# Optimization experiments

Hardware: AMD Instinct MI355X
Metric: run time of the kernel (lower is better)

Reference implementation:

```python
import jax, jax.numpy as jnp
import numpy as np

N_NODES = 100000


def _sage_conv(x, src, dst, W_l, b_l, W_r, n_nodes):
    # mean-aggregate neighbor features: messages flow src -> dst
    msg = x[src]                                              # [E, d]
    agg_sum = jax.ops.segment_sum(msg, dst, num_segments=n_nodes)   # [N, d]
    cnt = jax.ops.segment_sum(jnp.ones((src.shape[0],), x.dtype), dst,
                              num_segments=n_nodes)           # [N]
    agg = agg_sum / jnp.maximum(cnt, 1.0)[:, None]            # mean, 0 for isolated nodes
    return agg @ W_l + b_l + x @ W_r                          # lin_l(agg) + lin_r(x)


def setup_inputs() -> dict:
    key = jax.random.key(0)
    ks = jax.random.split(key, 8)
    in_c, hid_c, out_c = 64, 128, 64
    n_edges = 1000000
    x = jax.random.normal(ks[0], (N_NODES, in_c), dtype=jnp.float32)
    edge_index = jax.random.randint(ks[1], (2, n_edges), 0, N_NODES, dtype=jnp.int32)
    def glorot(k, shape):
        lim = float(np.sqrt(6.0 / (shape[0] + shape[1])))
        return jax.random.uniform(k, shape, jnp.float32, -lim, lim)
    return {
        "x": x,
        "edge_index": edge_index,
        "W_l1": glorot(ks[2], (in_c, hid_c)),
        "b_l1": jnp.zeros((hid_c,), jnp.float32),
        "W_r1": glorot(ks[3], (in_c, hid_c)),
        "W_l2": glorot(ks[4], (hid_c, out_c)),
        "b_l2": jnp.zeros((out_c,), jnp.float32),
        "W_r2": glorot(ks[5], (hid_c, out_c)),
    }


def reference(x, edge_index, W_l1, b_l1, W_r1, W_l2, b_l2, W_r2):
    src, dst = edge_index[0], edge_index[1]
    # eval mode: dropout(p=0.5) is identity
    h = _sage_conv(x, src, dst, W_l1, b_l1, W_r1, N_NODES)
    h = jax.nn.relu(h)
    out = _sage_conv(h, src, dst, W_l2, b_l2, W_r2, N_NODES)
    return out
```

## Files before the change

kernel.cpp:

```cpp
#include <hip/hip_runtime.h>


#define NPB 128
#define NBK 782
#define BCAP_E 1600
#define BCAP_S 2048

typedef __attribute__((ext_vector_type(8))) short bf16x8;
typedef __attribute__((ext_vector_type(4))) float f32x4;
typedef __attribute__((ext_vector_type(4))) int int4v;

__device__ __forceinline__ float bf2f(unsigned short u) {
  return __uint_as_float(((unsigned)u) << 16);
}
__device__ __forceinline__ unsigned short f2bf(float f) {
  unsigned x = __float_as_uint(f);
  x += 0x7fffu + ((x >> 16) & 1u);
  return (unsigned short)(x >> 16);
}

__global__ __launch_bounds__(256) void prep_all(
    const float* __restrict__ x, unsigned short* __restrict__ xb, int total4,
    const float* __restrict__ Wl1, const float* __restrict__ Wr1,
    const float* __restrict__ Wl2, const float* __restrict__ Wr2,
    unsigned short* __restrict__ Wt1, unsigned short* __restrict__ Wcat,
    unsigned short* __restrict__ tzero,
    const int* __restrict__ src, const int* __restrict__ dst,
    int* __restrict__ gcnt, int* __restrict__ ebuf, int e,
    int n, int CB) {
  __shared__ int lcnt[NBK], lbase[NBK];
  int b = blockIdx.x;
  if (b < CB) {
    int i = b * 256 + threadIdx.x;
    if (i < total4) {
      float4 v = ((const float4*)x)[i];
      ushort4 o;
      o.x = f2bf(v.x); o.y = f2bf(v.y); o.z = f2bf(v.z); o.w = f2bf(v.w);
      ((ushort4*)xb)[i] = o;
    }
    return;
  }
  if (b < CB + 128) {
    int o = (b - CB) * 256 + threadIdx.x;
    if (o < 16384) {
      int m = o >> 13, rem = o & 8191;
      int col = rem >> 6, k = rem & 63;
      const float* W = m ? Wr1 : Wl1;
      Wt1[o] = f2bf(W[k * 128 + col]);
    } else {
      int o2 = o - 16384;
      int col = o2 >> 7, k = o2 & 127;
      float v = (col < 64) ? Wl2[k * 64 + col] : Wr2[k * 64 + col - 64];
      Wcat[o2] = f2bf(v);
    }
    return;
  }
  if (b < CB + 129) {
    if (threadIdx.x < 32) {
      ((unsigned*)(xb + (size_t)n * 64))[threadIdx.x] = 0;
      ((unsigned*)(tzero + (size_t)n * 64))[threadIdx.x] = 0;
    }
    return;
  }
  int bb = b - (CB + 129);
  for (int i = threadIdx.x; i < NBK; i += 256) lcnt[i] = 0;
  __syncthreads();
  int pk[16], bk[16];
  int nv = 0;
  int base = bb * 4096 + threadIdx.x * 4;
#pragma unroll
  for (int c = 0; c < 4; ++c) {
    int i = base + c * 1024;
    if (i + 4 <= e) {
      int4v sv = *(const int4v*)(src + i);
      int4v dv = *(const int4v*)(dst + i);
#pragma unroll
      for (int j = 0; j < 4; ++j) {
        bk[nv] = dv[j] >> 7;
        pk[nv] = ((dv[j] & 127) << 17) | sv[j];
        ++nv;
      }
    } else if (i < e) {
      for (int i2 = i; i2 < e; ++i2) {
        int dj = dst[i2], sj = src[i2];
        bk[nv] = dj >> 7;
        pk[nv] = ((dj & 127) << 17) | sj;
        ++nv;
      }
    }
  }
  for (int k = 0; k < nv; ++k) atomicAdd(&lcnt[bk[k]], 1);
  __syncthreads();
  for (int i = threadIdx.x; i < NBK; i += 256) {
    lbase[i] = atomicAdd(&gcnt[i], lcnt[i]);
    lcnt[i] = 0;
  }
  __syncthreads();
  for (int k = 0; k < nv; ++k) {
    int off = lbase[bk[k]] + atomicAdd(&lcnt[bk[k]], 1);
    if (off < BCAP_E) ebuf[bk[k] * BCAP_E + off] = pk[k];
  }
}

__global__ __launch_bounds__(512) void sort_gather_gemm1(
    const unsigned short* __restrict__ xb, const int* __restrict__ gcnt,
    const int* __restrict__ ebuf, const unsigned short* __restrict__ Wt1,
    const float* __restrict__ b1,
    int* __restrict__ srcS, int* __restrict__ nstart, int* __restrict__ ncnt,
    unsigned short* __restrict__ h, int n) {
  __shared__ unsigned short sW[16384];
  __shared__ unsigned short sA[8192];
  __shared__ int sorted[BCAP_S];
  __shared__ int cnt[NPB], cur[NPB], st[NPB + 1];
  int tid = threadIdx.x, lane = tid & 63, wid = tid >> 6;
  int l15 = lane & 15, g = lane >> 4;
  int b = blockIdx.x;

#pragma unroll
  for (int it = 0; it < 4; ++it) {
    int i = it * 512 + tid;
    int byte = i << 4;
    int col = (byte >> 7) & 127;
    int koff = (byte & 127) ^ ((col & 7) << 4);
    int dstb = (byte & ~127) | koff;
    bf16x8 v = *(const bf16x8*)(Wt1 + i * 8);
    *(bf16x8*)((char*)sW + dstb) = v;
  }
  float bj[8];
#pragma unroll
  for (int cb = 0; cb < 8; ++cb) bj[cb] = b1[cb * 16 + l15];

  if (tid < NPB) { cnt[tid] = 0; cur[tid] = 0; }
  __syncthreads();
  int ecnt = min(gcnt[b], BCAP_E);
  const int* eb = ebuf + b * BCAP_E;
  for (int i = tid; i < ecnt; i += 512) atomicAdd(&cnt[eb[i] >> 17], 1);
  __syncthreads();
  if (wid == 0) {
    int i0 = (cnt[lane] + 3) & ~3, i1 = (cnt[64 + lane] + 3) & ~3;
#pragma unroll
    for (int off = 1; off < 64; off <<= 1) {
      int u = __shfl_up(i0, off);
      if (lane >= off) i0 += u;
    }
    int t0 = __shfl(i0, 63);
#pragma unroll
    for (int off = 1; off < 64; off <<= 1) {
      int u = __shfl_up(i1, off);
      if (lane >= off) i1 += u;
    }
    st[lane + 1] = i0;
    st[64 + lane + 1] = t0 + i1;
    if (lane == 0) st[0] = 0;
  }
  __syncthreads();
  for (int i = tid; i < ecnt; i += 512) {
    int pk = eb[i];
    int dl = pk >> 17;
    int pos = st[dl] + atomicAdd(&cur[dl], 1);
    if (pos < BCAP_S) sorted[pos] = pk & 0x1FFFF;
  }
  __syncthreads();
  if (tid < NPB) {
    int c = cnt[tid], p = (c + 3) & ~3;
    int base = st[tid];
    for (int k = c; k < p; ++k)
      if (base + k < BCAP_S) sorted[base + k] = n;
    int node = b * NPB + tid;
    if (node < n) {
      nstart[node] = b * BCAP_S + base;
      ncnt[node] = c;
    }
  }
  __syncthreads();
  int total = min(st[NPB], BCAP_S);
  for (int i = tid; i < total; i += 512) srcS[b * BCAP_S + i] = sorted[i];

  {
    int half32 = lane & 32;
    int hlane = lane & 31;
    int gg = hlane >> 3;
    int ch8 = lane & 7;
#pragma unroll 1
    for (int pass = 0; pass < 8; ++pass) {
      int dl = pass * 16 + wid * 2 + (lane >> 5);
      int s = st[dl], c = cnt[dl];
      int dpad = (c + 3) & ~3;
      float acc[8];
#pragma unroll
      for (int j = 0; j < 8; ++j) acc[j] = 0.f;
      int nit = dpad >> 2;
      int nitw = max(nit, __shfl_xor(nit, 32));
      int idx = (s + hlane < BCAP_S) ? sorted[s + hlane] : n;
      bf16x8 cch[8];
#pragma unroll
      for (int u = 0; u < 8; ++u) {
        if (u < nitw) {
          int r = u * 4 + gg;
          int sidx = __shfl(idx, half32 + r);
          if (u < nit) cch[u] = *(const bf16x8*)(xb + (size_t)sidx * 64 + ch8 * 8);
        }
      }
#pragma unroll
      for (int u = 0; u < 8; ++u) {
        if (u < nitw && u < nit) {
#pragma unroll
          for (int j = 0; j < 8; ++j) acc[j] += bf2f((unsigned short)cch[u][j]);
        }
      }
      for (int b0 = 32; b0 < dpad; b0 += 32) {
        int idx2 = (s + b0 + hlane < BCAP_S) ? sorted[s + b0 + hlane] : n;
#pragma unroll
        for (int u = 0; u < 8; ++u) {
          int r = u * 4 + gg;
          if (b0 + r < dpad) {
            int sidx = __shfl(idx2, half32 + r);
            bf16x8 v = *(const bf16x8*)(xb + (size_t)sidx * 64 + ch8 * 8);
#pragma unroll
            for (int j = 0; j < 8; ++j) acc[j] += bf2f((unsigned short)v[j]);
          }
        }
      }
#pragma unroll
      for (int m = 8; m < 32; m <<= 1) {
#pragma unroll
        for (int j = 0; j < 8; ++j) acc[j] += __shfl_xor(acc[j], m);
      }
      if (hlane < 8) {
        float inv = 1.f / (float)max(c, 1);
        bf16x8 o;
#pragma unroll
        for (int j = 0; j < 8; ++j) o[j] = (short)f2bf(acc[j] * inv);
        int byte = dl * 128 + ((ch8 * 16) ^ ((dl & 7) << 4));
        *(bf16x8*)((char*)sA + byte) = o;
      }
    }
  }
  __syncthreads();

  int rowl = wid * 16 + l15;
  int growbase = b * 128 + wid * 16;
  size_t cr = (size_t)min(growbase + l15, n - 1);

  f32x4 acc[8];
#pragma unroll
  for (int cb = 0; cb < 8; ++cb) acc[cb] = (f32x4){0.f, 0.f, 0.f, 0.f};

#pragma unroll
  for (int m = 0; m < 2; ++m) {
#pragma unroll
    for (int s = 0; s < 2; ++s) {
      int ko = s * 64 + g * 16;
      bf16x8 a;
      if (m == 0) {
        int koff = ko ^ ((rowl & 7) << 4);
        a = *(const bf16x8*)((const char*)sA + rowl * 128 + koff);
      } else {
        a = *(const bf16x8*)((const char*)xb + cr * 128 + ko);
      }
#pragma unroll
      for (int cb = 0; cb < 8; ++cb) {
        int col = cb * 16 + l15;
        int koff = ko ^ ((col & 7) << 4);
        bf16x8 bb = *(const bf16x8*)((const char*)sW + m * 16384 + col * 128 + koff);
        acc[cb] = __builtin_amdgcn_mfma_f32_16x16x32_bf16(a, bb, acc[cb], 0, 0, 0);
      }
    }
  }
  int rb = growbase + g * 4;
#pragma unroll
  for (int r = 0; r < 4; ++r) {
    int row = rb + r;
    if (row < n) {
      unsigned short* hp = h + (size_t)row * 128 + l15;
#pragma unroll
      for (int cb = 0; cb < 8; ++cb) {
        float v = fmaxf(acc[cb][r] + bj[cb], 0.f);
        hp[cb * 16] = f2bf(v);
      }
    }
  }
}

__global__ __launch_bounds__(256) void gemm2_mfma(
    const unsigned short* __restrict__ h, const unsigned short* __restrict__ Wcat,
    const float* __restrict__ b2, unsigned short* __restrict__ t,
    float* __restrict__ outp, int n) {
  __shared__ unsigned short sW[16384];
  int tid = threadIdx.x;
  int lane = tid & 63, wid = tid >> 6;
  int l15 = lane & 15, g = lane >> 4;
#pragma unroll
  for (int it = 0; it < 8; ++it) {
    int i = it * 256 + tid;
    int byte = i << 4;
    int col = byte >> 8;
    int koff = (byte & 255) ^ ((col & 15) << 4);
    int dstb = (byte & ~255) | koff;
    bf16x8 v = *(const bf16x8*)(Wcat + i * 8);
    *(bf16x8*)((char*)sW + dstb) = v;
  }
  float bj[4];
#pragma unroll
  for (int cb = 0; cb < 4; ++cb) bj[cb] = b2[cb * 16 + l15];
  __syncthreads();

  int rowbase = blockIdx.x * 128 + wid * 32;
  int r0 = rowbase + l15, r1 = r0 + 16;
  size_t cr0 = (size_t)min(r0, n - 1), cr1 = (size_t)min(r1, n - 1);

  f32x4 acc[2][8];
#pragma unroll
  for (int fr = 0; fr < 2; ++fr)
#pragma unroll
    for (int cb = 0; cb < 8; ++cb) acc[fr][cb] = (f32x4){0.f, 0.f, 0.f, 0.f};

  const char* hb = (const char*)h;
#pragma unroll
  for (int s = 0; s < 4; ++s) {
    int ko = s * 64 + g * 16;
    bf16x8 a0 = *(const bf16x8*)(hb + cr0 * 256 + ko);
    bf16x8 a1 = *(const bf16x8*)(hb + cr1 * 256 + ko);
#pragma unroll
    for (int cb = 0; cb < 8; ++cb) {
      int col = cb * 16 + l15;
      int koff = ko ^ ((col & 15) << 4);
      bf16x8 b = *(const bf16x8*)((const char*)sW + col * 256 + koff);
      acc[0][cb] = __builtin_amdgcn_mfma_f32_16x16x32_bf16(a0, b, acc[0][cb], 0, 0, 0);
      acc[1][cb] = __builtin_amdgcn_mfma_f32_16x16x32_bf16(a1, b, acc[1][cb], 0, 0, 0);
    }
  }
#pragma unroll
  for (int fr = 0; fr < 2; ++fr) {
    int rb = rowbase + fr * 16 + g * 4;
#pragma unroll
    for (int r = 0; r < 4; ++r) {
      int row = rb + r;
      if (row < n) {
#pragma unroll
        for (int cb = 0; cb < 4; ++cb)
          t[(size_t)row * 64 + cb * 16 + l15] = f2bf(acc[fr][cb][r]);
#pragma unroll
        for (int cb = 0; cb < 4; ++cb)
          outp[(size_t)row * 64 + cb * 16 + l15] = acc[fr][cb + 4][r] + bj[cb];
      }
    }
  }
}

__device__ __forceinline__ void gather2(
    const unsigned short* __restrict__ feat, const int* __restrict__ srcS,
    int s, int dpad, int lane, float* acc) {
  int half32 = lane & 32;
  int hlane = lane & 31;
  int g = hlane >> 3;
  int ch8 = lane & 7;
#pragma unroll
  for (int j = 0; j < 8; ++j) acc[j] = 0.f;
  int nit = dpad >> 2;
  int nitw = max(nit, __shfl_xor(nit, 32));
  int idx = srcS[s + hlane];
  bf16x8 c[8];
#pragma unroll
  for (int u = 0; u < 8; ++u) {
    if (u < nitw) {
      int r = u * 4 + g;
      int sidx = __shfl(idx, half32 + r);
      if (u < nit) c[u] = *(const bf16x8*)(feat + (size_t)sidx * 64 + ch8 * 8);
    }
  }
#pragma unroll
  for (int u = 0; u < 8; ++u) {
    if (u < nitw && u < nit) {
#pragma unroll
      for (int j = 0; j < 8; ++j) acc[j] += bf2f((unsigned short)c[u][j]);
    }
  }
  for (int b0 = 32; b0 < dpad; b0 += 32) {
    int idx2 = srcS[s + b0 + hlane];
#pragma unroll
    for (int u = 0; u < 8; ++u) {
      int r = u * 4 + g;
      if (b0 + r < dpad) {
        int sidx = __shfl(idx2, half32 + r);
        bf16x8 v = *(const bf16x8*)(feat + (size_t)sidx * 64 + ch8 * 8);
#pragma unroll
        for (int j = 0; j < 8; ++j) acc[j] += bf2f((unsigned short)v[j]);
      }
    }
  }
#pragma unroll
  for (int m = 8; m < 32; m <<= 1) {
#pragma unroll
    for (int j = 0; j < 8; ++j) acc[j] += __shfl_xor(acc[j], m);
  }
}

__global__ __launch_bounds__(256) void agg_add_fast(
    const unsigned short* __restrict__ feat, const int* __restrict__ nstart,
    const int* __restrict__ ncnt, const int* __restrict__ srcS,
    float* __restrict__ outp, int n) {
  int lane = threadIdx.x & 63, wid = threadIdx.x >> 6;
  int half = lane >> 5;
  int node = (blockIdx.x * 4 + wid) * 2 + half;
  bool live = node < n;
  int cn = live ? node : n - 1;
  int s = nstart[cn];
  int c = ncnt[cn];
  int dpad = (c + 3) & ~3;
  float acc[8];
  gather2(feat, srcS, s, dpad, lane, acc);
  float inv = 1.f / (float)max(c, 1);
  if ((lane & 31) < 8 && live) {
    float4* op = (float4*)(outp + (size_t)node * 64 + (lane & 7) * 8);
    float4 o0 = op[0], o1 = op[1];
    o0.x += acc[0] * inv; o0.y += acc[1] * inv;
    o0.z += acc[2] * inv; o0.w += acc[3] * inv;
    o1.x += acc[4] * inv; o1.y += acc[5] * inv;
    o1.z += acc[6] * inv; o1.w += acc[7] * inv;
    op[0] = o0; op[1] = o1;
  }
}

extern "C" void kernel_launch(void* const* d_in, const int* in_sizes, int n_in,
                              void* d_out, int out_size, void* d_ws, size_t ws_size,
                              hipStream_t stream) {
  const float* x   = (const float*)d_in[0];
  const int*   ei  = (const int*)d_in[1];
  const float* Wl1 = (const float*)d_in[2];
  const float* b1  = (const float*)d_in[3];
  const float* Wr1 = (const float*)d_in[4];
  const float* Wl2 = (const float*)d_in[5];
  const float* b2  = (const float*)d_in[6];
  const float* Wr2 = (const float*)d_in[7];
  float* out = (float*)d_out;

  const int n = in_sizes[0] / 64;
  const int e = in_sizes[1] / 2;
  const int* src = ei;
  const int* dst = ei + e;

  char* ws = (char*)d_ws;
  size_t off = 0;
  auto take = [&](size_t bytes) { void* p = ws + off; off = (off + bytes + 255) & ~(size_t)255; return p; };
  int*            gcnt   = (int*)take((size_t)NBK * 4);
  int*            ebuf   = (int*)take((size_t)NBK * BCAP_E * 4);
  int*            srcS   = (int*)take((size_t)NBK * BCAP_S * 4 + 256);
  int*            nstart = (int*)take((size_t)n * 4);
  int*            ncnt   = (int*)take((size_t)n * 4);
  unsigned short* xb     = (unsigned short*)take(((size_t)n + 1) * 64 * 2);
  unsigned short* t      = (unsigned short*)take(((size_t)n + 1) * 64 * 2);
  unsigned short* h      = (unsigned short*)take((size_t)n * 128 * 2);
  unsigned short* Wt1    = (unsigned short*)take(16384 * 2);
  unsigned short* Wcat   = (unsigned short*)take(16384 * 2);

  const int total4 = n * 64 / 4;
  const int CB = (total4 + 255) / 256;
  const int EB2 = (e + 4095) / 4096;

  (void)hipMemsetAsync(gcnt, 0, (size_t)NBK * 4, stream);
  prep_all<<<CB + 129 + EB2, 256, 0, stream>>>(x, xb, total4,
                                               Wl1, Wr1, Wl2, Wr2, Wt1, Wcat,
                                               t, src, dst, gcnt, ebuf, e, n, CB);
  sort_gather_gemm1<<<NBK, 512, 0, stream>>>(xb, gcnt, ebuf, Wt1, b1,
                                             srcS, nstart, ncnt, h, n);
  gemm2_mfma<<<NBK, 256, 0, stream>>>(h, Wcat, b2, t, out, n);
  agg_add_fast<<<(n + 7) / 8, 256, 0, stream>>>(t, nstart, ncnt, srcS, out, n);
}
```

Measured before the change: 124.0 us.

## Split bucketize and per-bucket sort into separate kernels, fold memset into prep

```diff
diff --git a/kernel.cpp b/kernel.cpp
--- a/kernel.cpp
+++ b/kernel.cpp
@@ -19,16 +19,13 @@
   return (unsigned short)(x >> 16);
 }
 
-__global__ __launch_bounds__(256) void prep_all(
+__global__ __launch_bounds__(256) void fused_misc(
     const float* __restrict__ x, unsigned short* __restrict__ xb, int total4,
     const float* __restrict__ Wl1, const float* __restrict__ Wr1,
     const float* __restrict__ Wl2, const float* __restrict__ Wr2,
     unsigned short* __restrict__ Wt1, unsigned short* __restrict__ Wcat,
-    unsigned short* __restrict__ tzero,
-    const int* __restrict__ src, const int* __restrict__ dst,
-    int* __restrict__ gcnt, int* __restrict__ ebuf, int e,
+    int* __restrict__ gcnt, unsigned short* __restrict__ tzero,
     int n, int CB) {
-  __shared__ int lcnt[NBK], lbase[NBK];
   int b = blockIdx.x;
   if (b < CB) {
     int i = b * 256 + threadIdx.x;
@@ -38,9 +35,7 @@
       o.x = f2bf(v.x); o.y = f2bf(v.y); o.z = f2bf(v.z); o.w = f2bf(v.w);
       ((ushort4*)xb)[i] = o;
     }
-    return;
-  }
-  if (b < CB + 128) {
+  } else if (b < CB + 128) {
     int o = (b - CB) * 256 + threadIdx.x;
     if (o < 16384) {
       int m = o >> 13, rem = o & 8191;
@@ -53,21 +48,24 @@
       float v = (col < 64) ? Wl2[k * 64 + col] : Wr2[k * 64 + col - 64];
       Wcat[o2] = f2bf(v);
     }
-    return;
-  }
-  if (b < CB + 129) {
+  } else {
+    for (int i = threadIdx.x; i < NBK; i += 256) gcnt[i] = 0;
     if (threadIdx.x < 32) {
       ((unsigned*)(xb + (size_t)n * 64))[threadIdx.x] = 0;
       ((unsigned*)(tzero + (size_t)n * 64))[threadIdx.x] = 0;
     }
-    return;
-  }
-  int bb = b - (CB + 129);
+  }
+}
+
+__global__ __launch_bounds__(256) void bucketize(
+    const int* __restrict__ src, const int* __restrict__ dst,
+    int* __restrict__ gcnt, int* __restrict__ ebuf, int e) {
+  __shared__ int lcnt[NBK], lbase[NBK];
   for (int i = threadIdx.x; i < NBK; i += 256) lcnt[i] = 0;
   __syncthreads();
   int pk[16], bk[16];
   int nv = 0;
-  int base = bb * 4096 + threadIdx.x * 4;
+  int base = blockIdx.x * 4096 + threadIdx.x * 4;
 #pragma unroll
   for (int c = 0; c < 4; ++c) {
     int i = base + c * 1024;
@@ -102,16 +100,69 @@
   }
 }
 
-__global__ __launch_bounds__(512) void sort_gather_gemm1(
-    const unsigned short* __restrict__ xb, const int* __restrict__ gcnt,
-    const int* __restrict__ ebuf, const unsigned short* __restrict__ Wt1,
-    const float* __restrict__ b1,
+__global__ __launch_bounds__(256) void sort_write(
+    const int* __restrict__ gcnt, const int* __restrict__ ebuf,
     int* __restrict__ srcS, int* __restrict__ nstart, int* __restrict__ ncnt,
+    int n) {
+  __shared__ int cnt[NPB], cur[NPB], st[NPB + 1], sorted[BCAP_S];
+  int tid = threadIdx.x, lane = tid & 63, wid = tid >> 6;
+  int b = blockIdx.x;
+  if (tid < NPB) { cnt[tid] = 0; cur[tid] = 0; }
+  __syncthreads();
+  int ecnt = min(gcnt[b], BCAP_E);
+  const int* eb = ebuf + b * BCAP_E;
+  for (int i = tid; i < ecnt; i += 256) atomicAdd(&cnt[eb[i] >> 17], 1);
+  __syncthreads();
+  if (wid == 0) {
+    int i0 = (cnt[lane] + 3) & ~3, i1 = (cnt[64 + lane] + 3) & ~3;
+#pragma unroll
+    for (int off = 1; off < 64; off <<= 1) {
+      int u = __shfl_up(i0, off);
+      if (lane >= off) i0 += u;
+    }
+    int t0 = __shfl(i0, 63);
+#pragma unroll
+    for (int off = 1; off < 64; off <<= 1) {
+      int u = __shfl_up(i1, off);
+      if (lane >= off) i1 += u;
+    }
+    st[lane + 1] = i0;
+    st[64 + lane + 1] = t0 + i1;
+    if (lane == 0) st[0] = 0;
+  }
+  __syncthreads();
+  for (int i = tid; i < ecnt; i += 256) {
+    int pk = eb[i];
+    int dl = pk >> 17;
+    int pos = st[dl] + atomicAdd(&cur[dl], 1);
+    if (pos < BCAP_S) sorted[pos] = pk & 0x1FFFF;
+  }
+  __syncthreads();
+  if (tid < NPB) {
+    int c = cnt[tid], p = (c + 3) & ~3;
+    int base = st[tid];
+    for (int k = c; k < p; ++k)
+      if (base + k < BCAP_S) sorted[base + k] = n;
+  }
+  __syncthreads();
+  int total = min(st[NPB], BCAP_S);
+  for (int i = tid; i < total; i += 256) srcS[b * BCAP_S + i] = sorted[i];
+  if (tid < NPB) {
+    int node = b * NPB + tid;
+    if (node < n) {
+      nstart[node] = b * BCAP_S + st[tid];
+      ncnt[node] = cnt[tid];
+    }
+  }
+}
+
+__global__ __launch_bounds__(512) void gather_gemm1(
+    const unsigned short* __restrict__ xb, const int* __restrict__ nstart,
+    const int* __restrict__ ncnt, const int* __restrict__ srcS,
+    const unsigned short* __restrict__ Wt1, const float* __restrict__ b1,
     unsigned short* __restrict__ h, int n) {
   __shared__ unsigned short sW[16384];
   __shared__ unsigned short sA[8192];
-  __shared__ int sorted[BCAP_S];
-  __shared__ int cnt[NPB], cur[NPB], st[NPB + 1];
   int tid = threadIdx.x, lane = tid & 63, wid = tid >> 6;
   int l15 = lane & 15, g = lane >> 4;
   int b = blockIdx.x;
@@ -130,52 +181,6 @@
 #pragma unroll
   for (int cb = 0; cb < 8; ++cb) bj[cb] = b1[cb * 16 + l15];
 
-  if (tid < NPB) { cnt[tid] = 0; cur[tid] = 0; }
-  __syncthreads();
-  int ecnt = min(gcnt[b], BCAP_E);
-  const int* eb = ebuf + b * BCAP_E;
-  for (int i = tid; i < ecnt; i += 512) atomicAdd(&cnt[eb[i] >> 17], 1);
-  __syncthreads();
-  if (wid == 0) {
-    int i0 = (cnt[lane] + 3) & ~3, i1 = (cnt[64 + lane] + 3) & ~3;
-#pragma unroll
-    for (int off = 1; off < 64; off <<= 1) {
-      int u = __shfl_up(i0, off);
-      if (lane >= off) i0 += u;
-    }
-    int t0 = __shfl(i0, 63);
-#pragma unroll
-    for (int off = 1; off < 64; off <<= 1) {
-      int u = __shfl_up(i1, off);
-      if (lane >= off) i1 += u;
-    }
-    st[lane + 1] = i0;
-    st[64 + lane + 1] = t0 + i1;
-    if (lane == 0) st[0] = 0;
-  }
-  __syncthreads();
-  for (int i = tid; i < ecnt; i += 512) {
-    int pk = eb[i];
-    int dl = pk >> 17;
-    int pos = st[dl] + atomicAdd(&cur[dl], 1);
-    if (pos < BCAP_S) sorted[pos] = pk & 0x1FFFF;
-  }
-  __syncthreads();
-  if (tid < NPB) {
-    int c = cnt[tid], p = (c + 3) & ~3;
-    int base = st[tid];
-    for (int k = c; k < p; ++k)
-      if (base + k < BCAP_S) sorted[base + k] = n;
-    int node = b * NPB + tid;
-    if (node < n) {
-      nstart[node] = b * BCAP_S + base;
-      ncnt[node] = c;
-    }
-  }
-  __syncthreads();
-  int total = min(st[NPB], BCAP_S);
-  for (int i = tid; i < total; i += 512) srcS[b * BCAP_S + i] = sorted[i];
-
   {
     int half32 = lane & 32;
     int hlane = lane & 31;
@@ -184,14 +189,17 @@
 #pragma unroll 1
     for (int pass = 0; pass < 8; ++pass) {
       int dl = pass * 16 + wid * 2 + (lane >> 5);
-      int s = st[dl], c = cnt[dl];
+      int node = b * NPB + dl;
+      int s, c;
+      if (node < n) { s = nstart[node]; c = ncnt[node]; }
+      else          { s = b * BCAP_S;   c = 0; }
       int dpad = (c + 3) & ~3;
       float acc[8];
 #pragma unroll
       for (int j = 0; j < 8; ++j) acc[j] = 0.f;
       int nit = dpad >> 2;
       int nitw = max(nit, __shfl_xor(nit, 32));
-      int idx = (s + hlane < BCAP_S) ? sorted[s + hlane] : n;
+      int idx = srcS[s + hlane];
       bf16x8 cch[8];
 #pragma unroll
       for (int u = 0; u < 8; ++u) {
@@ -209,7 +217,7 @@
         }
       }
       for (int b0 = 32; b0 < dpad; b0 += 32) {
-        int idx2 = (s + b0 + hlane < BCAP_S) ? sorted[s + b0 + hlane] : n;
+        int idx2 = srcS[s + b0 + hlane];
 #pragma unroll
         for (int u = 0; u < 8; ++u) {
           int r = u * 4 + gg;
@@ -456,14 +464,15 @@
 
   const int total4 = n * 64 / 4;
   const int CB = (total4 + 255) / 256;
-  const int EB2 = (e + 4095) / 4096;
-
-  (void)hipMemsetAsync(gcnt, 0, (size_t)NBK * 4, stream);
-  prep_all<<<CB + 129 + EB2, 256, 0, stream>>>(x, xb, total4,
+
+  fused_misc<<<CB + 128 + 1, 256, 0, stream>>>(x, xb, total4,
                                                Wl1, Wr1, Wl2, Wr2, Wt1, Wcat,
-                                               t, src, dst, gcnt, ebuf, e, n, CB);
-  sort_gather_gemm1<<<NBK, 512, 0, stream>>>(xb, gcnt, ebuf, Wt1, b1,
-                                             srcS, nstart, ncnt, h, n);
+                                               gcnt, t, n, CB);
+  bucketize<<<(e + 4095) / 4096, 256, 0, stream>>>(src, dst, gcnt, ebuf, e);
+  sort_write<<<NBK, 256, 0, stream>>>(gcnt, ebuf, srcS, nstart, ncnt, n);
+
+  gather_gemm1<<<NBK, 512, 0, stream>>>(xb, nstart, ncnt, srcS, Wt1, b1, h, n);
+
   gemm2_mfma<<<NBK, 256, 0, stream>>>(h, Wcat, b2, t, out, n);
   agg_add_fast<<<(n + 7) / 8, 256, 0, stream>>>(t, nstart, ncnt, srcS, out, n);
 }
```

Result: no change. 123.5 us (-0.4%).
